# Kernel tuning notes

Measured on AMD Instinct MI355X. Metric: run time of the kernel, lower is better.

## Reference

```python
import jax, jax.numpy as jnp
import numpy as np

DIM = 512
EPS = 1e-08
LN_EPS = 1e-05  # torch LayerNorm default


def layer_norm(x, g, b):
    mu = jnp.mean(x, axis=-1, keepdims=True)
    var = jnp.mean(jnp.square(x - mu), axis=-1, keepdims=True)
    return (x - mu) * jax.lax.rsqrt(var + LN_EPS) * g + b


def setup_inputs() -> dict:
    key = jax.random.key(0)
    ks = jax.random.split(key, 10)
    B, NQ, NK, D = 8, 1024, 2048, DIM
    s = 1.0 / np.sqrt(D)
    return {
        "inputs": jax.random.normal(ks[0], (B, NQ, D), jnp.float32),
        "context": jax.random.normal(ks[1], (B, NK, D), jnp.float32),
        "ln_in_g": jnp.ones((D,), jnp.float32),
        "ln_in_b": jnp.zeros((D,), jnp.float32),
        "ln_ctx_g": jnp.ones((D,), jnp.float32),
        "ln_ctx_b": jnp.zeros((D,), jnp.float32),
        "Wq": jax.random.uniform(ks[2], (D, D), jnp.float32, -s, s),
        "bq": jax.random.uniform(ks[3], (D,), jnp.float32, -s, s),
        "Wk": jax.random.uniform(ks[4], (D, D), jnp.float32, -s, s),
        "bk": jax.random.uniform(ks[5], (D,), jnp.float32, -s, s),
        "Wv": jax.random.uniform(ks[6], (D, D), jnp.float32, -s, s),
        "bv": jax.random.uniform(ks[7], (D,), jnp.float32, -s, s),
    }


def reference(inputs, context, ln_in_g, ln_in_b, ln_ctx_g, ln_ctx_b, Wq, bq, Wk, bk, Wv, bv):
    x = layer_norm(inputs, ln_in_g, ln_in_b)
    c = layer_norm(context, ln_ctx_g, ln_ctx_b)
    q = x @ Wq.T + bq  # [B, Nq, D]
    k = c @ Wk.T + bk  # [B, Nk, D]
    v = c @ Wv.T + bv  # [B, Nk, D]
    scale = DIM ** (-0.5)
    dots = jnp.einsum('bid,bjd->bij', q, k) * scale  # [B, Nq, Nk]
    attn = jax.nn.softmax(dots, axis=1) + EPS  # softmax over query axis
    attn = attn / jnp.sum(attn, axis=2, keepdims=True)  # renorm over key axis
    updates = jnp.einsum('bjd,bij->bid', v, attn)
    return updates
```

## Files before the change

### kernel.cpp

```cpp
#include <hip/hip_runtime.h>

using u16 = unsigned short;
typedef __attribute__((ext_vector_type(8))) short short8;
typedef __attribute__((ext_vector_type(4))) float floatx4;

#define NQ 1024
#define NK 2048
#define DD 512

__device__ __forceinline__ u16 f2bf(float f) {
  union { float f; unsigned u; } x; x.f = f;
  unsigned r = (x.u + 0x7fffu + ((x.u >> 16) & 1u)) >> 16;
  return (u16)r;
}
__device__ __forceinline__ float bf2f(u16 u) {
  union { unsigned u; float f; } x; x.u = ((unsigned)u) << 16; return x.f;
}
__device__ __forceinline__ float wave_sum(float v) {
#pragma unroll
  for (int off = 32; off > 0; off >>= 1) v += __shfl_down(v, off, 64);
  return v;
}
__device__ __forceinline__ void gload16(const u16* g, const u16* l) {
  __builtin_amdgcn_global_load_lds(
      (const __attribute__((address_space(1))) void*)g,
      (__attribute__((address_space(3))) void*)l, 16, 0, 0);
}

__global__ __launch_bounds__(256) void ln_prep(
    const float* __restrict__ X1, const float* __restrict__ G1,
    const float* __restrict__ B1, u16* __restrict__ Y1,
    const float* __restrict__ X2, const float* __restrict__ G2,
    const float* __restrict__ B2, u16* __restrict__ Y2,
    const float* __restrict__ Wq, const float* __restrict__ Wk,
    const float* __restrict__ Wv, u16* __restrict__ wqb,
    u16* __restrict__ wkb, u16* __restrict__ wvb, float* __restrict__ Zero) {
  const int bx = blockIdx.x;
  const int t = threadIdx.x;
  if (bx >= 6144) {
    int e = bx - 6144;
    if (e < 768) {
      const float* src = e < 256 ? Wq : (e < 512 ? Wk : Wv);
      u16* dst = e < 256 ? wqb : (e < 512 ? wkb : wvb);
      int i = ((e & 255) * 256 + t) * 4;
      float4 v = *(const float4*)(src + i);
      ushort4 o;
      o.x = f2bf(v.x); o.y = f2bf(v.y); o.z = f2bf(v.z); o.w = f2bf(v.w);
      *(ushort4*)(dst + i) = o;
    } else {
      int i = ((e - 768) * 256 + t) * 4;
      float4 z = {0.f, 0.f, 0.f, 0.f};
      *(float4*)(Zero + i) = z;
    }
    return;
  }
  const int wave = t >> 6, lane = t & 63;
  int row = bx * 4 + wave;
  const float *X, *G, *Bv; u16* Y;
  if (row < 8192) { X = X1; G = G1; Bv = B1; Y = Y1; }
  else { row -= 8192; X = X2; G = G2; Bv = B2; Y = Y2; }
  const float4* Xp = (const float4*)(X + (long)row * DD);
  float4 v0 = Xp[lane * 2], v1 = Xp[lane * 2 + 1];
  float s = v0.x + v0.y + v0.z + v0.w + v1.x + v1.y + v1.z + v1.w;
  float ss = v0.x * v0.x + v0.y * v0.y + v0.z * v0.z + v0.w * v0.w +
             v1.x * v1.x + v1.y * v1.y + v1.z * v1.z + v1.w * v1.w;
  s = wave_sum(s);  s = __shfl(s, 0, 64);
  ss = wave_sum(ss); ss = __shfl(ss, 0, 64);
  float mu = s * (1.f / DD);
  float var = ss * (1.f / DD) - mu * mu;
  float rs = rsqrtf(var + 1e-5f);
  const float4* Gp = (const float4*)G;
  const float4* Bp = (const float4*)Bv;
  float4 g0 = Gp[lane * 2], g1 = Gp[lane * 2 + 1];
  float4 b0 = Bp[lane * 2], b1 = Bp[lane * 2 + 1];
  short8 o;
  o[0] = (short)f2bf((v0.x - mu) * rs * g0.x + b0.x);
  o[1] = (short)f2bf((v0.y - mu) * rs * g0.y + b0.y);
  o[2] = (short)f2bf((v0.z - mu) * rs * g0.z + b0.z);
  o[3] = (short)f2bf((v0.w - mu) * rs * g0.w + b0.w);
  o[4] = (short)f2bf((v1.x - mu) * rs * g1.x + b1.x);
  o[5] = (short)f2bf((v1.y - mu) * rs * g1.y + b1.y);
  o[6] = (short)f2bf((v1.z - mu) * rs * g1.z + b1.z);
  o[7] = (short)f2bf((v1.w - mu) * rs * g1.w + b1.w);
  *(short8*)(Y + (long)row * DD + lane * 8) = o;
}

__global__ __launch_bounds__(256) void gemm_proj(
    const u16* __restrict__ A1, const u16* __restrict__ W1,
    const float* __restrict__ b1, u16* __restrict__ C1,
    const u16* __restrict__ A2, const u16* __restrict__ W2,
    const float* __restrict__ b2, u16* __restrict__ C2) {
  __shared__ u16 smem[16384];
  u16* lA = smem;
  u16* lB = smem + 8192;
  const u16 *A, *B; const float* bias; u16* Cout;
  int m0 = blockIdx.x * 128;
  if (blockIdx.x < 64) { A = A1; B = W1; bias = b1; Cout = C1; }
  else { A = A2; B = W2; bias = b2; Cout = C2; m0 = (blockIdx.x - 64) * 128; }
  const int n0 = blockIdx.y * 128;
  const int t = threadIdx.x, wave = t >> 6, lane = t & 63;
  const int fm = lane & 15, fq = lane >> 4;
  const int wm = (wave >> 1) * 64, wn = (wave & 1) * 64;

  const int srow = t >> 3;
  const int swz = ((t & 7) ^ (srow & 7)) * 8;
  const u16* gA = A + (long)(m0 + srow) * 512 + swz;
  const u16* gB = B + (long)(n0 + srow) * 512 + swz;
  u16* dA = lA + wave * 512;
  u16* dB = lB + wave * 512;

  floatx4 acc[4][4];
#pragma unroll
  for (int x = 0; x < 4; ++x)
#pragma unroll
    for (int y = 0; y < 4; ++y) { floatx4 z = {0.f, 0.f, 0.f, 0.f}; acc[x][y] = z; }

#pragma unroll 1
  for (int kt = 0; kt < 8; ++kt) {
    gload16(gA, dA);
    gload16(gA + 32L * 512, dA + 2048);
    gload16(gA + 64L * 512, dA + 4096);
    gload16(gA + 96L * 512, dA + 6144);
    gload16(gB, dB);
    gload16(gB + 32L * 512, dB + 2048);
    gload16(gB + 64L * 512, dB + 4096);
    gload16(gB + 96L * 512, dB + 6144);
    gA += 64; gB += 64;
    __syncthreads();
#pragma unroll
    for (int ks = 0; ks < 2; ++ks) {
      short8 af[4], bfr[4];
      const int csl = ((ks * 4 + fq) ^ (fm & 7)) * 8;
#pragma unroll
      for (int x = 0; x < 4; ++x)
        af[x] = *(const short8*)&lA[(wm + x * 16 + fm) * 64 + csl];
#pragma unroll
      for (int y = 0; y < 4; ++y)
        bfr[y] = *(const short8*)&lB[(wn + y * 16 + fm) * 64 + csl];
#pragma unroll
      for (int x = 0; x < 4; ++x)
#pragma unroll
        for (int y = 0; y < 4; ++y)
          acc[x][y] = __builtin_amdgcn_mfma_f32_16x16x32_bf16(af[x], bfr[y], acc[x][y], 0, 0, 0);
    }
    __syncthreads();
  }

  float bs[4];
#pragma unroll
  for (int y = 0; y < 4; ++y) bs[y] = bias[n0 + wn + y * 16 + fm];
#pragma unroll
  for (int x = 0; x < 4; ++x)
#pragma unroll
    for (int y = 0; y < 4; ++y) {
      const int cblk = (wn >> 4) + y;
#pragma unroll
      for (int r = 0; r < 4; ++r) {
        int rowl = wm + x * 16 + fq * 4 + r;
        smem[rowl * 128 + ((cblk ^ fq) * 16) + fm] = f2bf(acc[x][y][r] + bs[y]);
      }
    }
  __syncthreads();
#pragma unroll
  for (int p = 0; p < 8; ++p) {
    int rowl = p * 16 + (t >> 4);
    int c = t & 15;
    int q = (rowl >> 2) & 3;
    short8 v = *(const short8*)&smem[rowl * 128 + (((c >> 1) ^ q) * 16) + (c & 1) * 8];
    *(short8*)(Cout + (long)(m0 + rowl) * 512 + n0 + c * 8) = v;
  }
}

__global__ __launch_bounds__(256) void qk_vproj(
    const u16* __restrict__ qb, const u16* __restrict__ kb,
    u16* __restrict__ E, float* __restrict__ Z,
    const u16* __restrict__ wvb, const u16* __restrict__ cb,
    const float* __restrict__ bv, u16* __restrict__ vT,
    float* __restrict__ colV, float scale) {
  __shared__ u16 smem[16384];
  __shared__ float colred[128];
  u16* lA = smem;
  u16* lB = smem + 8192;

  const int bx = blockIdx.x;
  const bool is_qk = bx < 1024;
  const u16 *A, *B;
  int m0, n0, b;
  if (is_qk) {
    b = bx & 7;
    n0 = ((bx >> 3) & 15) * 128;
    m0 = (bx >> 7) * 128;
    A = qb + (long)b * (1024L * 512);
    B = kb + (long)b * (2048L * 512);
  } else {
    int e = bx - 1024;
    m0 = (e & 3) * 128;
    n0 = (e >> 2) * 128;
    b = 0;
    A = wvb;
    B = cb;
  }
  const int t = threadIdx.x, wave = t >> 6, lane = t & 63;
  const int fm = lane & 15, fq = lane >> 4;
  const int wm = (wave >> 1) * 64, wn = (wave & 1) * 64;

  const int srow = t >> 3;
  const int swz = ((t & 7) ^ (srow & 7)) * 8;
  const u16* gA = A + (long)(m0 + srow) * 512 + swz;
  const u16* gB = B + (long)(n0 + srow) * 512 + swz;
  u16* dA = lA + wave * 512;
  u16* dB = lB + wave * 512;

  floatx4 acc[4][4];
#pragma unroll
  for (int x = 0; x < 4; ++x)
#pragma unroll
    for (int y = 0; y < 4; ++y) { floatx4 z = {0.f, 0.f, 0.f, 0.f}; acc[x][y] = z; }

#pragma unroll 1
  for (int kt = 0; kt < 8; ++kt) {
    gload16(gA, dA);
    gload16(gA + 32L * 512, dA + 2048);
    gload16(gA + 64L * 512, dA + 4096);
    gload16(gA + 96L * 512, dA + 6144);
    gload16(gB, dB);
    gload16(gB + 32L * 512, dB + 2048);
    gload16(gB + 64L * 512, dB + 4096);
    gload16(gB + 96L * 512, dB + 6144);
    gA += 64; gB += 64;
    __syncthreads();
#pragma unroll
    for (int ks = 0; ks < 2; ++ks) {
      short8 af[4], bfr[4];
      const int csl = ((ks * 4 + fq) ^ (fm & 7)) * 8;
#pragma unroll
      for (int x = 0; x < 4; ++x)
        af[x] = *(const short8*)&lA[(wm + x * 16 + fm) * 64 + csl];
#pragma unroll
      for (int y = 0; y < 4; ++y)
        bfr[y] = *(const short8*)&lB[(wn + y * 16 + fm) * 64 + csl];
#pragma unroll
      for (int x = 0; x < 4; ++x)
#pragma unroll
        for (int y = 0; y < 4; ++y)
          acc[x][y] = __builtin_amdgcn_mfma_f32_16x16x32_bf16(af[x], bfr[y], acc[x][y], 0, 0, 0);
    }
    __syncthreads();
  }

  if (is_qk) {
    float s4[4] = {0.f, 0.f, 0.f, 0.f};
#pragma unroll
    for (int x = 0; x < 4; ++x)
#pragma unroll
      for (int y = 0; y < 4; ++y) {
        const int cblk = (wn >> 4) + y;
#pragma unroll
        for (int r = 0; r < 4; ++r) {
          int rowl = wm + x * 16 + fq * 4 + r;
          float e = __expf(acc[x][y][r] * scale);
          s4[y] += e;
          smem[rowl * 128 + ((cblk ^ fq) * 16) + fm] = f2bf(e);
        }
      }
#pragma unroll
    for (int y = 0; y < 4; ++y) {
      s4[y] += __shfl_xor(s4[y], 16, 64);
      s4[y] += __shfl_xor(s4[y], 32, 64);
    }
    if (t < 128) colred[t] = 0.f;
    __syncthreads();
    u16* Eg = E + (long)b * (1024L * 2048);
#pragma unroll
    for (int p = 0; p < 8; ++p) {
      int rowl = p * 16 + (t >> 4);
      int c = t & 15;
      int q = (rowl >> 2) & 3;
      short8 v = *(const short8*)&smem[rowl * 128 + (((c >> 1) ^ q) * 16) + (c & 1) * 8];
      *(short8*)(Eg + (long)(m0 + rowl) * 2048 + n0 + c * 8) = v;
    }
    if (fq == 0) {
#pragma unroll
      for (int y = 0; y < 4; ++y) atomicAdd(&colred[wn + y * 16 + fm], s4[y]);
    }
    __syncthreads();
    if (t < 128) atomicAdd(&Z[b * 2048 + n0 + t], colred[t]);
  } else {
    const int bb = n0 >> 11;
    const int j0c = n0 & 2047;
    float bsr[4][4];
#pragma unroll
    for (int x = 0; x < 4; ++x)
#pragma unroll
      for (int r = 0; r < 4; ++r)
        bsr[x][r] = bv[m0 + wm + x * 16 + fq * 4 + r];
    float rs[4][4];
#pragma unroll
    for (int x = 0; x < 4; ++x)
#pragma unroll
      for (int r = 0; r < 4; ++r) rs[x][r] = 0.f;
#pragma unroll
    for (int x = 0; x < 4; ++x)
#pragma unroll
      for (int y = 0; y < 4; ++y) {
        const int cblk = (wn >> 4) + y;
#pragma unroll
        for (int r = 0; r < 4; ++r) {
          int rowl = wm + x * 16 + fq * 4 + r;
          float val = acc[x][y][r] + bsr[x][r];
          rs[x][r] += val;
          smem[rowl * 128 + ((cblk ^ fq) * 16) + fm] = f2bf(val);
        }
      }
    __syncthreads();
    u16* Cg = vT + (long)bb * (512L * 2048) + j0c;
#pragma unroll
    for (int p = 0; p < 8; ++p) {
      int rowl = p * 16 + (t >> 4);
      int c = t & 15;
      int q = (rowl >> 2) & 3;
      short8 v = *(const short8*)&smem[rowl * 128 + (((c >> 1) ^ q) * 16) + (c & 1) * 8];
      *(short8*)(Cg + (long)(m0 + rowl) * 2048 + c * 8) = v;
    }
#pragma unroll
    for (int x = 0; x < 4; ++x)
#pragma unroll
      for (int r = 0; r < 4; ++r) {
        float s = rs[x][r];
        s += __shfl_xor(s, 1, 64);
        s += __shfl_xor(s, 2, 64);
        s += __shfl_xor(s, 4, 64);
        s += __shfl_xor(s, 8, 64);
        if (fm == 0)
          atomicAdd(&colV[bb * 512 + m0 + wm + x * 16 + fq * 4 + r], s);
      }
  }
}

__global__ __launch_bounds__(256) void scaleV(u16* __restrict__ vT,
                                              const float* __restrict__ Z) {
  const long f = ((long)blockIdx.x * 256 + threadIdx.x) * 8;
  const int b = (int)(f >> 20);
  const float* zp = Z + b * 2048 + (int)(f & 2047);
  short8 v = *(const short8*)(vT + f);
  short8 o;
#pragma unroll
  for (int k = 0; k < 8; ++k)
    o[k] = (short)f2bf(bf2f((u16)v[k]) * __builtin_amdgcn_rcpf(zp[k]));
  *(short8*)(vT + f) = o;
}

__global__ __launch_bounds__(256) void gemm_pv(const u16* __restrict__ E,
    const u16* __restrict__ V, const float* __restrict__ colV,
    const float* __restrict__ Z, float* __restrict__ out) {
  __shared__ u16 smem[8192];
  __shared__ u16 sZb[2048];
  u16* lA = smem;
  u16* lB = smem + 4096;
  const int id = blockIdx.x;
  const int b = id & 7;
  const int m0 = ((id >> 3) & 15) * 64, n0 = (id >> 7) * 64;
  const int t = threadIdx.x, wave = t >> 6, lane = t & 63;
  const int fm = lane & 15, fq = lane >> 4;
  const int wm = (wave >> 1) * 32, wn = (wave & 1) * 32;

  {
    int i = t * 8;
    float4 z0 = *(const float4*)(Z + b * 2048 + i);
    float4 z1 = *(const float4*)(Z + b * 2048 + i + 4);
    short8 o;
    o[0] = (short)f2bf(__builtin_amdgcn_rcpf(z0.x));
    o[1] = (short)f2bf(__builtin_amdgcn_rcpf(z0.y));
    o[2] = (short)f2bf(__builtin_amdgcn_rcpf(z0.z));
    o[3] = (short)f2bf(__builtin_amdgcn_rcpf(z0.w));
    o[4] = (short)f2bf(__builtin_amdgcn_rcpf(z1.x));
    o[5] = (short)f2bf(__builtin_amdgcn_rcpf(z1.y));
    o[6] = (short)f2bf(__builtin_amdgcn_rcpf(z1.z));
    o[7] = (short)f2bf(__builtin_amdgcn_rcpf(z1.w));
    *(short8*)&sZb[i] = o;
  }

  const int srow = t >> 3;
  const int swz = ((t & 7) ^ (srow & 7)) * 8;
  const u16* gA = E + (long)b * (1024L * 2048) + (long)(m0 + srow) * 2048 + swz;
  const u16* gB = V + (long)b * (512L * 2048) + (long)(n0 + srow) * 2048 + swz;
  u16* dA = lA + wave * 512;
  u16* dB = lB + wave * 512;

  floatx4 acc[2][2];
  floatx4 accR[2];
#pragma unroll
  for (int x = 0; x < 2; ++x) {
    floatx4 z = {0.f, 0.f, 0.f, 0.f};
    accR[x] = z;
#pragma unroll
    for (int y = 0; y < 2; ++y) acc[x][y] = z;
  }

#pragma unroll 1
  for (int kt = 0; kt < 32; ++kt) {
    gload16(gA, dA);
    gload16(gA + 32L * 2048, dA + 2048);
    gload16(gB, dB);
    gload16(gB + 32L * 2048, dB + 2048);
    gA += 64; gB += 64;
    __syncthreads();
#pragma unroll
    for (int ks = 0; ks < 2; ++ks) {
      short8 af[2], bfr[2];
      const int chunk = ks * 4 + fq;
      const int csl = (chunk ^ (fm & 7)) * 8;
#pragma unroll
      for (int x = 0; x < 2; ++x)
        af[x] = *(const short8*)&lA[(wm + x * 16 + fm) * 64 + csl];
#pragma unroll
      for (int y = 0; y < 2; ++y)
        bfr[y] = *(const short8*)&lB[(wn + y * 16 + fm) * 64 + csl];
      short8 zf = *(const short8*)&sZb[kt * 64 + chunk * 8];
#pragma unroll
      for (int x = 0; x < 2; ++x) {
#pragma unroll
        for (int y = 0; y < 2; ++y)
          acc[x][y] = __builtin_amdgcn_mfma_f32_16x16x32_bf16(af[x], bfr[y], acc[x][y], 0, 0, 0);
        accR[x] = __builtin_amdgcn_mfma_f32_16x16x32_bf16(af[x], zf, accR[x], 0, 0, 0);
      }
    }
    __syncthreads();
  }

  float cv[2];
#pragma unroll
  for (int y = 0; y < 2; ++y) cv[y] = colV[b * 512 + n0 + wn + y * 16 + fm];
  float* sO = (float*)smem;
#pragma unroll
  for (int x = 0; x < 2; ++x)
#pragma unroll
    for (int r = 0; r < 4; ++r) {
      float invR = __builtin_amdgcn_rcpf(accR[x][r] + 2048.f * 1e-8f);
      int rowl = wm + x * 16 + fq * 4 + r;
#pragma unroll
      for (int y = 0; y < 2; ++y) {
        const int cblk = (wn >> 4) + y;
        sO[rowl * 64 + ((cblk ^ fq) * 16) + fm] =
            (acc[x][y][r] + 1e-8f * cv[y]) * invR;
      }
    }
  __syncthreads();
  float* og = out + (long)b * (1024L * 512);
#pragma unroll
  for (int p = 0; p < 4; ++p) {
    int rowl = p * 16 + (t >> 4);
    int c = t & 15;
    int q = (rowl >> 2) & 3;
    float4 v = *(const float4*)&sO[rowl * 64 + (((c >> 2) ^ q) * 16) + (c & 3) * 4];
    *(float4*)(og + (long)(m0 + rowl) * 512 + n0 + c * 4) = v;
  }
}

extern "C" void kernel_launch(void* const* d_in, const int* in_sizes, int n_in,
                              void* d_out, int out_size, void* d_ws, size_t ws_size,
                              hipStream_t stream) {
  const float* inputs  = (const float*)d_in[0];
  const float* context = (const float*)d_in[1];
  const float* ln_in_g = (const float*)d_in[2];
  const float* ln_in_b = (const float*)d_in[3];
  const float* ln_ctx_g = (const float*)d_in[4];
  const float* ln_ctx_b = (const float*)d_in[5];
  const float* Wq = (const float*)d_in[6];
  const float* bq = (const float*)d_in[7];
  const float* Wk = (const float*)d_in[8];
  const float* bk = (const float*)d_in[9];
  const float* Wv = (const float*)d_in[10];
  const float* bv = (const float*)d_in[11];
  float* out = (float*)d_out;

  u16* ws = (u16*)d_ws;
  u16* xb  = ws;
  u16* qb  = xb + 8192L * 512;
  u16* cb  = qb + 8192L * 512;
  u16* wqb = cb + 16384L * 512;
  u16* wkb = wqb + 512L * 512;
  u16* wvb = wkb + 512L * 512;
  u16* kb  = wvb + 512L * 512;
  u16* vTs = kb + 16384L * 512;
  u16* E   = vTs + 8L * 512 * 2048;
  float* Z    = (float*)(E + 8L * 1024 * 2048);
  float* colV = Z + 8L * 2048;

  const float scale = 0.04419417382415922f;

  ln_prep<<<6932, 256, 0, stream>>>(inputs, ln_in_g, ln_in_b, xb,
                                    context, ln_ctx_g, ln_ctx_b, cb,
                                    Wq, Wk, Wv, wqb, wkb, wvb, Z);
  gemm_proj<<<dim3(192, 4, 1), 256, 0, stream>>>(xb, wqb, bq, qb,
                                                 cb, wkb, bk, kb);
  qk_vproj<<<1536, 256, 0, stream>>>(qb, kb, E, Z, wvb, cb, bv, vTs,
                                     colV, scale);
  scaleV<<<4096, 256, 0, stream>>>(vTs, Z);
  gemm_pv<<<1024, 256, 0, stream>>>(E, vTs, colV, Z, out);
}
```

Measured before the change: 207.4 us.

## Fold 1/Z column scaling into PV A-fragments and drop scaleV kernel

Removes the separate scaleV pass over V and instead multiplies each E fragment by the per-column 1/Z inside gemm_pv before the MFMA, using a ones vector for the row-sum accumulation. It also drops the LDS-staged coalesced store of E and vT in qk_vproj, writing scalar bf16 values straight to global memory. This saves a kernel launch and a full read-write of V, but adds per-iteration VALU conversions in the PV inner loop and replaces 16-byte coalesced stores with scattered 2-byte stores for the large E matrix.

```diff
diff --git a/kernel.cpp b/kernel.cpp
--- a/kernel.cpp
+++ b/kernel.cpp
@@ -177,10 +177,9 @@
     const u16* __restrict__ wvb, const u16* __restrict__ cb,
     const float* __restrict__ bv, u16* __restrict__ vT,
     float* __restrict__ colV, float scale) {
-  __shared__ u16 smem[16384];
+  __shared__ u16 lA[128 * 64];
+  __shared__ u16 lB[128 * 64];
   __shared__ float colred[128];
-  u16* lA = smem;
-  u16* lB = smem + 8192;
 
   const int bx = blockIdx.x;
   const bool is_qk = bx < 1024;
@@ -250,19 +249,19 @@
 
   if (is_qk) {
     float s4[4] = {0.f, 0.f, 0.f, 0.f};
+    u16* Eg = E + (long)b * (1024L * 2048);
 #pragma unroll
     for (int x = 0; x < 4; ++x)
 #pragma unroll
-      for (int y = 0; y < 4; ++y) {
-        const int cblk = (wn >> 4) + y;
+      for (int y = 0; y < 4; ++y)
 #pragma unroll
         for (int r = 0; r < 4; ++r) {
-          int rowl = wm + x * 16 + fq * 4 + r;
+          int row = m0 + wm + x * 16 + fq * 4 + r;
+          int col = n0 + wn + y * 16 + fm;
           float e = __expf(acc[x][y][r] * scale);
           s4[y] += e;
-          smem[rowl * 128 + ((cblk ^ fq) * 16) + fm] = f2bf(e);
+          Eg[(long)row * 2048 + col] = f2bf(e);
         }
-      }
 #pragma unroll
     for (int y = 0; y < 4; ++y) {
       s4[y] += __shfl_xor(s4[y], 16, 64);
@@ -270,15 +269,6 @@
     }
     if (t < 128) colred[t] = 0.f;
     __syncthreads();
-    u16* Eg = E + (long)b * (1024L * 2048);
-#pragma unroll
-    for (int p = 0; p < 8; ++p) {
-      int rowl = p * 16 + (t >> 4);
-      int c = t & 15;
-      int q = (rowl >> 2) & 3;
-      short8 v = *(const short8*)&smem[rowl * 128 + (((c >> 1) ^ q) * 16) + (c & 1) * 8];
-      *(short8*)(Eg + (long)(m0 + rowl) * 2048 + n0 + c * 8) = v;
-    }
     if (fq == 0) {
 #pragma unroll
       for (int y = 0; y < 4; ++y) atomicAdd(&colred[wn + y * 16 + fm], s4[y]);
@@ -294,6 +284,7 @@
 #pragma unroll
       for (int r = 0; r < 4; ++r)
         bsr[x][r] = bv[m0 + wm + x * 16 + fq * 4 + r];
+    u16* Cg = vT + (long)bb * (512L * 2048) + j0c;
     float rs[4][4];
 #pragma unroll
     for (int x = 0; x < 4; ++x)
@@ -302,26 +293,15 @@
 #pragma unroll
     for (int x = 0; x < 4; ++x)
 #pragma unroll
-      for (int y = 0; y < 4; ++y) {
-        const int cblk = (wn >> 4) + y;
+      for (int y = 0; y < 4; ++y)
 #pragma unroll
         for (int r = 0; r < 4; ++r) {
-          int rowl = wm + x * 16 + fq * 4 + r;
+          int rowd = m0 + wm + x * 16 + fq * 4 + r;
+          int col = wn + y * 16 + fm;
           float val = acc[x][y][r] + bsr[x][r];
           rs[x][r] += val;
-          smem[rowl * 128 + ((cblk ^ fq) * 16) + fm] = f2bf(val);
+          Cg[(long)rowd * 2048 + col] = f2bf(val);
         }
-      }
-    __syncthreads();
-    u16* Cg = vT + (long)bb * (512L * 2048) + j0c;
-#pragma unroll
-    for (int p = 0; p < 8; ++p) {
-      int rowl = p * 16 + (t >> 4);
-      int c = t & 15;
-      int q = (rowl >> 2) & 3;
-      short8 v = *(const short8*)&smem[rowl * 128 + (((c >> 1) ^ q) * 16) + (c & 1) * 8];
-      *(short8*)(Cg + (long)(m0 + rowl) * 2048 + c * 8) = v;
-    }
 #pragma unroll
     for (int x = 0; x < 4; ++x)
 #pragma unroll
@@ -335,19 +315,6 @@
           atomicAdd(&colV[bb * 512 + m0 + wm + x * 16 + fq * 4 + r], s);
       }
   }
-}
-
-__global__ __launch_bounds__(256) void scaleV(u16* __restrict__ vT,
-                                              const float* __restrict__ Z) {
-  const long f = ((long)blockIdx.x * 256 + threadIdx.x) * 8;
-  const int b = (int)(f >> 20);
-  const float* zp = Z + b * 2048 + (int)(f & 2047);
-  short8 v = *(const short8*)(vT + f);
-  short8 o;
-#pragma unroll
-  for (int k = 0; k < 8; ++k)
-    o[k] = (short)f2bf(bf2f((u16)v[k]) * __builtin_amdgcn_rcpf(zp[k]));
-  *(short8*)(vT + f) = o;
 }
 
 __global__ __launch_bounds__(256) void gemm_pv(const u16* __restrict__ E,
@@ -387,6 +354,10 @@
   u16* dA = lA + wave * 512;
   u16* dB = lB + wave * 512;
 
+  short8 ones;
+#pragma unroll
+  for (int i = 0; i < 8; ++i) ones[i] = (short)0x3F80;
+
   floatx4 acc[2][2];
   floatx4 accR[2];
 #pragma unroll
@@ -417,12 +388,26 @@
       for (int y = 0; y < 2; ++y)
         bfr[y] = *(const short8*)&lB[(wn + y * 16 + fm) * 64 + csl];
       short8 zf = *(const short8*)&sZb[kt * 64 + chunk * 8];
+      float zff[8];
+#pragma unroll
+      for (int i = 0; i < 8; ++i) zff[i] = bf2f((u16)zf[i]);
+#pragma unroll
+      for (int x = 0; x < 2; ++x) {
+        short8 afs;
+#pragma unroll
+        for (int i = 0; i < 8; ++i) {
+          union { float f; unsigned u; } p;
+          p.f = bf2f((u16)af[x][i]) * zff[i];
+          afs[i] = (short)(p.u >> 16);
+        }
+        af[x] = afs;
+      }
 #pragma unroll
       for (int x = 0; x < 2; ++x) {
 #pragma unroll
         for (int y = 0; y < 2; ++y)
           acc[x][y] = __builtin_amdgcn_mfma_f32_16x16x32_bf16(af[x], bfr[y], acc[x][y], 0, 0, 0);
-        accR[x] = __builtin_amdgcn_mfma_f32_16x16x32_bf16(af[x], zf, accR[x], 0, 0, 0);
+        accR[x] = __builtin_amdgcn_mfma_f32_16x16x32_bf16(af[x], ones, accR[x], 0, 0, 0);
       }
     }
     __syncthreads();
@@ -496,6 +481,5 @@
                                                  cb, wkb, bk, kb);
   qk_vproj<<<1536, 256, 0, stream>>>(qb, kb, E, Z, wvb, cb, bv, vTs,
                                      colV, scale);
-  scaleV<<<4096, 256, 0, stream>>>(vTs, Z);
   gemm_pv<<<1024, 256, 0, stream>>>(E, vTs, colV, Z, out);
 }
```

Result: slower. 218.4 us (+5.3%).
